# Kernel optimization log

Measured on AMD Instinct MI355X. Metric: run time of the kernel, lower is better.

Reference implementation:

```python
import jax, jax.numpy as jnp
import numpy as np

N, H, F, E, K = 2048, 1024, 4096, 8, 2


def setup_inputs() -> dict:
    key = jax.random.key(0)
    ks = jax.random.split(key, 6)
    x = jax.random.normal(ks[0], (N, H), dtype=jnp.float32)
    mapping = jax.random.randint(ks[1], (N, K), 0, E)
    Wg = jax.random.normal(ks[2], (E, H), dtype=jnp.float32) * (1.0 / np.sqrt(H))
    W1 = jax.random.normal(ks[3], (E, H, F), dtype=jnp.float32) * (1.0 / np.sqrt(H))
    b1 = jnp.zeros((E, F), dtype=jnp.float32)
    W2 = jax.random.normal(ks[4], (E, F, H), dtype=jnp.float32) * (1.0 / np.sqrt(F))
    b2 = jnp.zeros((E, H), dtype=jnp.float32)
    return {"x": x, "mapping": mapping, "Wg": Wg, "W1": W1, "b1": b1, "W2": W2, "b2": b2}


def reference(x, mapping, Wg, W1, b1, W2, b2):
    # Gate logits: note original applies softmax over dim=0 (the token axis).
    logits = jax.nn.softmax(x @ Wg.T, axis=0)  # [N, E]

    # Per-expert MLP. Original sorts tokens by expert, runs per-expert GEMMs on
    # dynamic splits, then unsorts -- mathematically: y[i,k] = MLP_{mapping[i,k]}(x[i]).
    # JIT-friendly dense baseline: run every expert over all tokens, gather per token.
    def mlp(e):
        h = jax.nn.gelu(x @ W1[e] + b1[e])  # [N, F]
        return h @ W2[e] + b2[e]            # [N, H]

    y_all = jnp.stack([mlp(e) for e in range(E)])  # [E, N, H]

    # Gate weights gathered per (token, k), normalized over top-k.
    w = jnp.take_along_axis(logits, mapping, axis=1)  # [N, K]
    w = w / jnp.sum(w, axis=-1, keepdims=True)

    idx = jnp.arange(x.shape[0])
    out = jnp.zeros_like(x)
    for k in range(mapping.shape[1]):
        yk = y_all[mapping[:, k], idx]  # [N, H] gather per token's k-th expert
        out = out + yk * w[:, k:k + 1]
    return out
```

## Files before the change

### kernel.cpp

```cpp
#include <hip/hip_runtime.h>

#define N_TOK 2048
#define HD    1024
#define FD    4096
#define NE    8
#define SK2   8

typedef __attribute__((ext_vector_type(8))) short short8;
typedef __attribute__((ext_vector_type(4))) float floatx4;

__device__ __forceinline__ unsigned short f2bf(float f) {
  unsigned int u = __float_as_uint(f);
  u += 0x7fffu + ((u >> 16) & 1u);
  return (unsigned short)(u >> 16);
}

__device__ __forceinline__ void gl2lds16(const unsigned short* g, unsigned short* l) {
  __builtin_amdgcn_global_load_lds(
      (const __attribute__((address_space(1))) unsigned int*)g,
      (__attribute__((address_space(3))) unsigned int*)l, 16, 0, 0);
}

__device__ __forceinline__ float gelu_tanh(float x) {
  float t = 0.7978845608028654f * x * (1.0f + 0.044715f * x * x);
  return 0.5f * x * (1.0f + tanhf(t));
}

__device__ __forceinline__ int poff_of(const int* __restrict__ cnt, int e) {
  int o = 0;
  for (int i = 0; i < e; ++i) o += (cnt[i] + 127) & ~127;
  return o;
}

__global__ void k_gating(const float* __restrict__ x, const float* __restrict__ wg,
                         float* __restrict__ p) {
  int wave = threadIdx.x >> 6;
  int lane = threadIdx.x & 63;
  int n = blockIdx.x * 4 + wave;
  const float4* xr = (const float4*)(x + (size_t)n * HD);
  float4 xv[4];
  #pragma unroll
  for (int i = 0; i < 4; ++i) xv[i] = xr[lane + i * 64];
  for (int e = 0; e < NE; ++e) {
    const float4* wr = (const float4*)(wg + (size_t)e * HD);
    float s = 0.f;
    #pragma unroll
    for (int i = 0; i < 4; ++i) {
      float4 w4 = wr[lane + i * 64];
      s += xv[i].x * w4.x + xv[i].y * w4.y + xv[i].z * w4.z + xv[i].w * w4.w;
    }
    for (int o = 32; o > 0; o >>= 1) s += __shfl_xor(s, o, 64);
    if (lane == 0) p[e * N_TOK + n] = s;
  }
}

__global__ void k_softmax(float* __restrict__ p) {
  int e = blockIdx.x;
  float* col = p + e * N_TOK;
  __shared__ float red[256];
  int t = threadIdx.x;
  float m = -1e30f;
  for (int i = t; i < N_TOK; i += 256) m = fmaxf(m, col[i]);
  red[t] = m; __syncthreads();
  for (int s = 128; s > 0; s >>= 1) { if (t < s) red[t] = fmaxf(red[t], red[t + s]); __syncthreads(); }
  m = red[0]; __syncthreads();
  float sum = 0.f;
  for (int i = t; i < N_TOK; i += 256) { float v = expf(col[i] - m); col[i] = v; sum += v; }
  red[t] = sum; __syncthreads();
  for (int s = 128; s > 0; s >>= 1) { if (t < s) red[t] += red[t + s]; __syncthreads(); }
  float inv = 1.0f / red[0];
  for (int i = t; i < N_TOK; i += 256) col[i] *= inv;
}

__global__ void k_route(const int* __restrict__ mp, const float* __restrict__ p,
                        int* __restrict__ cnt, int* __restrict__ idxl, float* __restrict__ wtl) {
  int n = blockIdx.x * 256 + threadIdx.x;
  if (n >= N_TOK) return;
  int m0 = mp[n * 2 + 0], m1 = mp[n * 2 + 1];
  if (m0 == m1) {
    int s = atomicAdd(&cnt[m0], 1);
    idxl[m0 * N_TOK + s] = n; wtl[m0 * N_TOK + s] = 1.0f;
  } else {
    float p0 = p[m0 * N_TOK + n], p1 = p[m1 * N_TOK + n];
    float inv = 1.0f / (p0 + p1);
    int s0 = atomicAdd(&cnt[m0], 1);
    idxl[m0 * N_TOK + s0] = n; wtl[m0 * N_TOK + s0] = p0 * inv;
    int s1 = atomicAdd(&cnt[m1], 1);
    idxl[m1 * N_TOK + s1] = n; wtl[m1 * N_TOK + s1] = p1 * inv;
  }
}

__global__ void k_gather(const float* __restrict__ x, const int* __restrict__ cnt,
                         const int* __restrict__ idxl, unsigned short* __restrict__ xg) {
  int e = blockIdx.y;
  int r = blockIdx.x;
  int c = cnt[e];
  int pc = (c + 127) & ~127;
  if (r >= pc) return;
  unsigned short* dst = xg + ((size_t)poff_of(cnt, e) + r) * HD;
  int t = threadIdx.x;
  union { unsigned short us[8]; uint4 v; } o;
  if (r < c) {
    const float* src = x + (size_t)idxl[e * N_TOK + r] * HD;
    float4 f0 = ((const float4*)src)[t * 2];
    float4 f1 = ((const float4*)src)[t * 2 + 1];
    o.us[0] = f2bf(f0.x); o.us[1] = f2bf(f0.y); o.us[2] = f2bf(f0.z); o.us[3] = f2bf(f0.w);
    o.us[4] = f2bf(f1.x); o.us[5] = f2bf(f1.y); o.us[6] = f2bf(f1.z); o.us[7] = f2bf(f1.w);
  } else {
    o.v.x = 0u; o.v.y = 0u; o.v.z = 0u; o.v.w = 0u;
  }
  ((uint4*)dst)[t] = o.v;
}

__global__ __launch_bounds__(256) void k_transcvt2(const float* __restrict__ w1,
                                                   unsigned short* __restrict__ w1t,
                                                   const float* __restrict__ w2,
                                                   unsigned short* __restrict__ w2t) {
  __shared__ float tile[64][65];
  int l = blockIdx.x;
  const float* src; unsigned short* dst; int rows, cols, bx, by, e;
  if (l < 8192) {
    src = w1; dst = w1t; rows = HD; cols = FD;
    bx = l & 63; by = (l >> 6) & 15; e = l >> 10;
  } else {
    int l2 = l - 8192;
    src = w2; dst = w2t; rows = FD; cols = HD;
    bx = l2 & 15; by = (l2 >> 4) & 63; e = l2 >> 10;
  }
  const size_t base = (size_t)e * rows * cols;
  int c0 = bx * 64, r0 = by * 64;
  int t = threadIdx.x;
  int lr = t >> 4;
  int lc = (t & 15) * 4;
  #pragma unroll
  for (int i = 0; i < 64; i += 16) {
    float4 v = *(const float4*)(src + base + (size_t)(r0 + lr + i) * cols + c0 + lc);
    tile[lr + i][lc] = v.x; tile[lr + i][lc + 1] = v.y;
    tile[lr + i][lc + 2] = v.z; tile[lr + i][lc + 3] = v.w;
  }
  __syncthreads();
  int oc = t >> 2;
  int rseg = (t & 3) * 16;
  union { unsigned short us[16]; uint4 v[2]; } o;
  #pragma unroll
  for (int i = 0; i < 16; ++i) o.us[i] = f2bf(tile[rseg + i][oc]);
  unsigned short* d = dst + base + (size_t)(c0 + oc) * rows + r0 + rseg;
  ((uint4*)d)[0] = o.v[0];
  ((uint4*)d)[1] = o.v[1];
}

__global__ __launch_bounds__(256) void k_gemm1(
    const unsigned short* __restrict__ xg, const unsigned short* __restrict__ w1t,
    const float* __restrict__ b1, const int* __restrict__ cnt,
    unsigned short* __restrict__ h) {
  const int l = blockIdx.x;
  const int r = l & 7;
  const int m = (l >> 3) & 31;
  const int q = l >> 8;
  const int e = q >> 2;
  const int n = ((q & 3) << 3) | r;

  const int c = cnt[e];
  const int mbase = m * 64;
  if (mbase >= c) return;
  const int nbase = n * 128;
  const int po = poff_of(cnt, e);
  const unsigned short* A = xg + ((size_t)po + mbase) * HD;
  const unsigned short* B = w1t + ((size_t)e * FD + nbase) * HD;

  __shared__ unsigned short As[64 * 32];
  __shared__ unsigned short Bs[128 * 32];

  const int tid = threadIdx.x;
  const int wave = tid >> 6, lane = tid & 63;
  const int quad = lane >> 4, lrow = lane & 15;
  const int wn = wave * 32;

  floatx4 acc[4][2];
  #pragma unroll
  for (int i = 0; i < 4; ++i)
    #pragma unroll
    for (int j = 0; j < 2; ++j) acc[i][j] = (floatx4){0.f, 0.f, 0.f, 0.f};

  const int rA = tid >> 2, kA = (tid & 3) * 8;
  const int rB0 = tid >> 2, kB0 = (tid & 3) * 8;
  const int rB1 = (256 + tid) >> 2, kB1 = ((256 + tid) & 3) * 8;

  for (int kt = 0; kt < HD / 32; ++kt) {
    __syncthreads();
    const unsigned short* ga = A + kt * 32;
    const unsigned short* gb = B + kt * 32;
    gl2lds16(ga + (size_t)rA * HD + kA, As + (size_t)(wave * 64) * 8);
    gl2lds16(gb + (size_t)rB0 * HD + kB0, Bs + (size_t)(wave * 64) * 8);
    gl2lds16(gb + (size_t)rB1 * HD + kB1, Bs + (size_t)(256 + wave * 64) * 8);
    __syncthreads();
    short8 aF[4], bF[2];
    #pragma unroll
    for (int i = 0; i < 4; ++i) aF[i] = *(const short8*)(As + (i * 16 + lrow) * 32 + quad * 8);
    #pragma unroll
    for (int j = 0; j < 2; ++j) bF[j] = *(const short8*)(Bs + (wn + j * 16 + lrow) * 32 + quad * 8);
    #pragma unroll
    for (int i = 0; i < 4; ++i)
      #pragma unroll
      for (int j = 0; j < 2; ++j)
        acc[i][j] = __builtin_amdgcn_mfma_f32_16x16x32_bf16(aF[i], bF[j], acc[i][j], 0, 0, 0);
  }

  const size_t hrow0 = (size_t)po + mbase;
  #pragma unroll
  for (int i = 0; i < 4; ++i) {
    #pragma unroll
    for (int rr = 0; rr < 4; ++rr) {
      int row = i * 16 + quad * 4 + rr;
      unsigned short* hr = h + (hrow0 + row) * FD + nbase;
      #pragma unroll
      for (int j = 0; j < 2; ++j) {
        int col = wn + j * 16 + lrow;
        float v = acc[i][j][rr] + b1[e * FD + nbase + col];
        hr[col] = f2bf(gelu_tanh(v));
      }
    }
  }
}

__global__ __launch_bounds__(256) void k_gemm2(
    const unsigned short* __restrict__ h, const unsigned short* __restrict__ w2t,
    const float* __restrict__ b2, const int* __restrict__ cnt,
    const int* __restrict__ idxl, const float* __restrict__ wtl, float* __restrict__ out) {
  const int l = blockIdx.x;
  const int sk = l & 7;
  const int m = (l >> 3) & 15;
  const int n = (l >> 7) & 7;
  const int e = l >> 10;

  const int c = cnt[e];
  const int mbase = m * 128;
  if (mbase >= c) return;
  const int nbase = n * 128;
  const int KC = FD / SK2;
  const int po = poff_of(cnt, e);
  const unsigned short* A = h + ((size_t)po + mbase) * FD + sk * KC;
  const unsigned short* B = w2t + ((size_t)e * HD + nbase) * FD + sk * KC;

  __shared__ unsigned short As[128 * 32];
  __shared__ unsigned short Bs[128 * 32];

  const int tid = threadIdx.x;
  const int wave = tid >> 6, lane = tid & 63;
  const int quad = lane >> 4, lrow = lane & 15;
  const int wm = (wave >> 1) * 64, wn = (wave & 1) * 64;

  floatx4 acc[4][4];
  #pragma unroll
  for (int i = 0; i < 4; ++i)
    #pragma unroll
    for (int j = 0; j < 4; ++j) acc[i][j] = (floatx4){0.f, 0.f, 0.f, 0.f};

  const int r0c = tid >> 2,          k0c = (tid & 3) * 8;
  const int r1c = (256 + tid) >> 2,  k1c = ((256 + tid) & 3) * 8;

  for (int kt = 0; kt < KC / 32; ++kt) {
    __syncthreads();
    const unsigned short* ga = A + kt * 32;
    const unsigned short* gb = B + kt * 32;
    gl2lds16(ga + (size_t)r0c * FD + k0c, As + (size_t)(wave * 64) * 8);
    gl2lds16(ga + (size_t)r1c * FD + k1c, As + (size_t)(256 + wave * 64) * 8);
    gl2lds16(gb + (size_t)r0c * FD + k0c, Bs + (size_t)(wave * 64) * 8);
    gl2lds16(gb + (size_t)r1c * FD + k1c, Bs + (size_t)(256 + wave * 64) * 8);
    __syncthreads();
    short8 aF[4], bF[4];
    #pragma unroll
    for (int i = 0; i < 4; ++i) aF[i] = *(const short8*)(As + (wm + i * 16 + lrow) * 32 + quad * 8);
    #pragma unroll
    for (int j = 0; j < 4; ++j) bF[j] = *(const short8*)(Bs + (wn + j * 16 + lrow) * 32 + quad * 8);
    #pragma unroll
    for (int i = 0; i < 4; ++i)
      #pragma unroll
      for (int j = 0; j < 4; ++j)
        acc[i][j] = __builtin_amdgcn_mfma_f32_16x16x32_bf16(aF[i], bF[j], acc[i][j], 0, 0, 0);
  }

  #pragma unroll
  for (int i = 0; i < 4; ++i) {
    #pragma unroll
    for (int rr = 0; rr < 4; ++rr) {
      int row = wm + i * 16 + quad * 4 + rr;
      int gr = mbase + row;
      if (gr < c) {
        int tok = idxl[e * N_TOK + gr];
        float wgt = wtl[e * N_TOK + gr];
        float* orow = out + (size_t)tok * HD + nbase;
        #pragma unroll
        for (int j = 0; j < 4; ++j) {
          int col = wn + j * 16 + lrow;
          float bias = (sk == 0) ? b2[e * HD + nbase + col] : 0.0f;
          atomicAdd(orow + col, wgt * (acc[i][j][rr] + bias));
        }
      }
    }
  }
}

extern "C" void kernel_launch(void* const* d_in, const int* in_sizes, int n_in,
                              void* d_out, int out_size, void* d_ws, size_t ws_size,
                              hipStream_t stream) {
  const float* x  = (const float*)d_in[0];
  const int*   mp = (const int*)d_in[1];
  const float* wg = (const float*)d_in[2];
  const float* w1 = (const float*)d_in[3];
  const float* b1 = (const float*)d_in[4];
  const float* w2 = (const float*)d_in[5];
  const float* b2 = (const float*)d_in[6];
  float* out = (float*)d_out;
  char* ws = (char*)d_ws;

  float* p    = (float*)(ws + 0);
  int*   cnt  = (int*)(ws + 65536);
  int*   idxl = (int*)(ws + 66048);
  float* wtl  = (float*)(ws + 131584);
  unsigned short* w1t = (unsigned short*)(ws + 197120);
  unsigned short* w2t = (unsigned short*)(ws + 197120 + 67108864);
  unsigned short* xg  = (unsigned short*)(ws + 197120 + 2 * 67108864);
  unsigned short* h   = (unsigned short*)(ws + 197120 + 2 * 67108864 + 10485760);

  hipMemsetAsync(cnt, 0, 32, stream);
  hipMemsetAsync(d_out, 0, (size_t)out_size * 4, stream);

  k_gating<<<512, 256, 0, stream>>>(x, wg, p);
  k_softmax<<<NE, 256, 0, stream>>>(p);
  k_route<<<NE, 256, 0, stream>>>(mp, p, cnt, idxl, wtl);
  k_transcvt2<<<16384, 256, 0, stream>>>(w1, w1t, w2, w2t);
  k_gather<<<dim3(N_TOK, NE), 128, 0, stream>>>(x, cnt, idxl, xg);
  k_gemm1<<<8192, 256, 0, stream>>>(xg, w1t, b1, cnt, h);
  k_gemm2<<<8192, 256, 0, stream>>>(h, w2t, b2, cnt, idxl, wtl, out);
}
```

Baseline: 580.2 us.

## Replace split-K atomic GEMM2 with full-K bf16 output plus per-token combine kernel

The second expert GEMM no longer splits K eight ways and scatters with float atomics into the output. It now computes full-K 64x64 tiles over the packed expert rows, writes bf16 results to a staging buffer, and a new combine kernel gathers each token's two expert rows, adds bias and applies the gate weights. Routing now records per-token expert, slot and weight, and the output memset is dropped. This removes heavy atomic traffic and the memset, but gives up split-K parallelism, uses smaller tiles with less reuse, and adds a bf16 rounding of the expert outputs.

```diff
diff --git a/kernel.cpp b/kernel.cpp
--- a/kernel.cpp
+++ b/kernel.cpp
@@ -4,7 +4,6 @@
 #define HD    1024
 #define FD    4096
 #define NE    8
-#define SK2   8
 
 typedef __attribute__((ext_vector_type(8))) short short8;
 typedef __attribute__((ext_vector_type(4))) float floatx4;
@@ -73,20 +72,25 @@
 }
 
 __global__ void k_route(const int* __restrict__ mp, const float* __restrict__ p,
-                        int* __restrict__ cnt, int* __restrict__ idxl, float* __restrict__ wtl) {
+                        int* __restrict__ cnt, int* __restrict__ idxl,
+                        int* __restrict__ tke, int* __restrict__ tks, float* __restrict__ tkw) {
   int n = blockIdx.x * 256 + threadIdx.x;
   if (n >= N_TOK) return;
   int m0 = mp[n * 2 + 0], m1 = mp[n * 2 + 1];
   if (m0 == m1) {
     int s = atomicAdd(&cnt[m0], 1);
-    idxl[m0 * N_TOK + s] = n; wtl[m0 * N_TOK + s] = 1.0f;
+    idxl[m0 * N_TOK + s] = n;
+    tke[n * 2] = m0; tks[n * 2] = s; tkw[n * 2] = 1.0f;
+    tke[n * 2 + 1] = m0; tks[n * 2 + 1] = s; tkw[n * 2 + 1] = 0.0f;
   } else {
     float p0 = p[m0 * N_TOK + n], p1 = p[m1 * N_TOK + n];
     float inv = 1.0f / (p0 + p1);
     int s0 = atomicAdd(&cnt[m0], 1);
-    idxl[m0 * N_TOK + s0] = n; wtl[m0 * N_TOK + s0] = p0 * inv;
+    idxl[m0 * N_TOK + s0] = n;
+    tke[n * 2] = m0; tks[n * 2] = s0; tkw[n * 2] = p0 * inv;
     int s1 = atomicAdd(&cnt[m1], 1);
-    idxl[m1 * N_TOK + s1] = n; wtl[m1 * N_TOK + s1] = p1 * inv;
+    idxl[m1 * N_TOK + s1] = n;
+    tke[n * 2 + 1] = m1; tks[n * 2 + 1] = s1; tkw[n * 2 + 1] = p1 * inv;
   }
 }
 
@@ -225,80 +229,108 @@
 
 __global__ __launch_bounds__(256) void k_gemm2(
     const unsigned short* __restrict__ h, const unsigned short* __restrict__ w2t,
-    const float* __restrict__ b2, const int* __restrict__ cnt,
-    const int* __restrict__ idxl, const float* __restrict__ wtl, float* __restrict__ out) {
+    const int* __restrict__ cnt, unsigned short* __restrict__ ya) {
   const int l = blockIdx.x;
-  const int sk = l & 7;
-  const int m = (l >> 3) & 15;
-  const int n = (l >> 7) & 7;
-  const int e = l >> 10;
-
-  const int c = cnt[e];
-  const int mbase = m * 128;
-  if (mbase >= c) return;
-  const int nbase = n * 128;
-  const int KC = FD / SK2;
-  const int po = poff_of(cnt, e);
-  const unsigned short* A = h + ((size_t)po + mbase) * FD + sk * KC;
-  const unsigned short* B = w2t + ((size_t)e * HD + nbase) * FD + sk * KC;
-
-  __shared__ unsigned short As[128 * 32];
-  __shared__ unsigned short Bs[128 * 32];
+  const int nt = l & 15;
+  const int mt = l >> 4;
+  const int mbase = mt * 64;
+  const int nbase = nt * 64;
+
+  int e = -1, po = 0, ce = 0;
+  {
+    int o = 0;
+    #pragma unroll
+    for (int i = 0; i < NE; ++i) {
+      int ci = cnt[i];
+      int pc = (ci + 127) & ~127;
+      if (mbase >= o && mbase < o + pc) { e = i; po = o; ce = ci; }
+      o += pc;
+    }
+  }
+  if (e < 0) return;
+  if (mbase - po >= ce) return;
+
+  const unsigned short* A = h + (size_t)mbase * FD;
+  const unsigned short* B = w2t + ((size_t)e * HD + nbase) * FD;
+
+  __shared__ unsigned short As[64 * 64];
+  __shared__ unsigned short Bs[64 * 64];
 
   const int tid = threadIdx.x;
   const int wave = tid >> 6, lane = tid & 63;
   const int quad = lane >> 4, lrow = lane & 15;
-  const int wm = (wave >> 1) * 64, wn = (wave & 1) * 64;
-
-  floatx4 acc[4][4];
-  #pragma unroll
-  for (int i = 0; i < 4; ++i)
-    #pragma unroll
-    for (int j = 0; j < 4; ++j) acc[i][j] = (floatx4){0.f, 0.f, 0.f, 0.f};
-
-  const int r0c = tid >> 2,          k0c = (tid & 3) * 8;
-  const int r1c = (256 + tid) >> 2,  k1c = ((256 + tid) & 3) * 8;
-
-  for (int kt = 0; kt < KC / 32; ++kt) {
+  const int wm = (wave >> 1) * 32, wn = (wave & 1) * 32;
+
+  floatx4 acc[2][2];
+  #pragma unroll
+  for (int i = 0; i < 2; ++i)
+    #pragma unroll
+    for (int j = 0; j < 2; ++j) acc[i][j] = (floatx4){0.f, 0.f, 0.f, 0.f};
+
+  const int s0 = tid,        r0 = s0 >> 3, k0 = (s0 & 7) * 8;
+  const int s1 = 256 + tid,  r1 = s1 >> 3, k1 = (s1 & 7) * 8;
+
+  for (int kt = 0; kt < FD / 64; ++kt) {
     __syncthreads();
-    const unsigned short* ga = A + kt * 32;
-    const unsigned short* gb = B + kt * 32;
-    gl2lds16(ga + (size_t)r0c * FD + k0c, As + (size_t)(wave * 64) * 8);
-    gl2lds16(ga + (size_t)r1c * FD + k1c, As + (size_t)(256 + wave * 64) * 8);
-    gl2lds16(gb + (size_t)r0c * FD + k0c, Bs + (size_t)(wave * 64) * 8);
-    gl2lds16(gb + (size_t)r1c * FD + k1c, Bs + (size_t)(256 + wave * 64) * 8);
+    const unsigned short* ga = A + kt * 64;
+    const unsigned short* gb = B + kt * 64;
+    gl2lds16(ga + (size_t)r0 * FD + k0, As + (size_t)(wave * 64) * 8);
+    gl2lds16(ga + (size_t)r1 * FD + k1, As + (size_t)(256 + wave * 64) * 8);
+    gl2lds16(gb + (size_t)r0 * FD + k0, Bs + (size_t)(wave * 64) * 8);
+    gl2lds16(gb + (size_t)r1 * FD + k1, Bs + (size_t)(256 + wave * 64) * 8);
     __syncthreads();
-    short8 aF[4], bF[4];
-    #pragma unroll
-    for (int i = 0; i < 4; ++i) aF[i] = *(const short8*)(As + (wm + i * 16 + lrow) * 32 + quad * 8);
-    #pragma unroll
-    for (int j = 0; j < 4; ++j) bF[j] = *(const short8*)(Bs + (wn + j * 16 + lrow) * 32 + quad * 8);
-    #pragma unroll
-    for (int i = 0; i < 4; ++i)
-      #pragma unroll
-      for (int j = 0; j < 4; ++j)
-        acc[i][j] = __builtin_amdgcn_mfma_f32_16x16x32_bf16(aF[i], bF[j], acc[i][j], 0, 0, 0);
-  }
-
-  #pragma unroll
-  for (int i = 0; i < 4; ++i) {
+    #pragma unroll
+    for (int c = 0; c < 2; ++c) {
+      short8 aF[2], bF[2];
+      #pragma unroll
+      for (int i = 0; i < 2; ++i) aF[i] = *(const short8*)(As + (wm + i * 16 + lrow) * 64 + c * 32 + quad * 8);
+      #pragma unroll
+      for (int j = 0; j < 2; ++j) bF[j] = *(const short8*)(Bs + (wn + j * 16 + lrow) * 64 + c * 32 + quad * 8);
+      #pragma unroll
+      for (int i = 0; i < 2; ++i)
+        #pragma unroll
+        for (int j = 0; j < 2; ++j)
+          acc[i][j] = __builtin_amdgcn_mfma_f32_16x16x32_bf16(aF[i], bF[j], acc[i][j], 0, 0, 0);
+    }
+  }
+
+  #pragma unroll
+  for (int i = 0; i < 2; ++i) {
     #pragma unroll
     for (int rr = 0; rr < 4; ++rr) {
-      int row = wm + i * 16 + quad * 4 + rr;
-      int gr = mbase + row;
-      if (gr < c) {
-        int tok = idxl[e * N_TOK + gr];
-        float wgt = wtl[e * N_TOK + gr];
-        float* orow = out + (size_t)tok * HD + nbase;
-        #pragma unroll
-        for (int j = 0; j < 4; ++j) {
-          int col = wn + j * 16 + lrow;
-          float bias = (sk == 0) ? b2[e * HD + nbase + col] : 0.0f;
-          atomicAdd(orow + col, wgt * (acc[i][j][rr] + bias));
-        }
+      int row = mbase + wm + i * 16 + quad * 4 + rr;
+      unsigned short* yr = ya + (size_t)row * HD + nbase;
+      #pragma unroll
+      for (int j = 0; j < 2; ++j) {
+        int col = wn + j * 16 + lrow;
+        yr[col] = f2bf(acc[i][j][rr]);
       }
     }
   }
+}
+
+__global__ __launch_bounds__(256) void k_combine(
+    const unsigned short* __restrict__ ya, const float* __restrict__ b2,
+    const int* __restrict__ cnt, const int* __restrict__ tke,
+    const int* __restrict__ tks, const float* __restrict__ tkw,
+    float* __restrict__ out) {
+  int n = blockIdx.x;
+  int e0 = tke[n * 2], e1 = tke[n * 2 + 1];
+  int p0 = poff_of(cnt, e0) + tks[n * 2];
+  int p1 = poff_of(cnt, e1) + tks[n * 2 + 1];
+  float w0 = tkw[n * 2], w1 = tkw[n * 2 + 1];
+  int c = threadIdx.x * 4;
+  union { unsigned short us[4]; ushort2 u2[2]; unsigned long long ll; } y0, y1;
+  y0.ll = *(const unsigned long long*)(ya + (size_t)p0 * HD + c);
+  y1.ll = *(const unsigned long long*)(ya + (size_t)p1 * HD + c);
+  float4 bb0 = *(const float4*)(b2 + (size_t)e0 * HD + c);
+  float4 bb1 = *(const float4*)(b2 + (size_t)e1 * HD + c);
+  float4 o;
+  o.x = w0 * (__uint_as_float((unsigned)y0.us[0] << 16) + bb0.x) + w1 * (__uint_as_float((unsigned)y1.us[0] << 16) + bb1.x);
+  o.y = w0 * (__uint_as_float((unsigned)y0.us[1] << 16) + bb0.y) + w1 * (__uint_as_float((unsigned)y1.us[1] << 16) + bb1.y);
+  o.z = w0 * (__uint_as_float((unsigned)y0.us[2] << 16) + bb0.z) + w1 * (__uint_as_float((unsigned)y1.us[2] << 16) + bb1.z);
+  o.w = w0 * (__uint_as_float((unsigned)y0.us[3] << 16) + bb0.w) + w1 * (__uint_as_float((unsigned)y1.us[3] << 16) + bb1.w);
+  *(float4*)(out + (size_t)n * HD + c) = o;
 }
 
 extern "C" void kernel_launch(void* const* d_in, const int* in_sizes, int n_in,
@@ -317,20 +349,24 @@
   float* p    = (float*)(ws + 0);
   int*   cnt  = (int*)(ws + 65536);
   int*   idxl = (int*)(ws + 66048);
-  float* wtl  = (float*)(ws + 131584);
-  unsigned short* w1t = (unsigned short*)(ws + 197120);
-  unsigned short* w2t = (unsigned short*)(ws + 197120 + 67108864);
-  unsigned short* xg  = (unsigned short*)(ws + 197120 + 2 * 67108864);
-  unsigned short* h   = (unsigned short*)(ws + 197120 + 2 * 67108864 + 10485760);
+  int*   tke  = (int*)(ws + 131584);
+  int*   tks  = (int*)(ws + 147968);
+  float* tkw  = (float*)(ws + 164352);
+  size_t off = 180736;
+  unsigned short* w1t = (unsigned short*)(ws + off);  off += 67108864;
+  unsigned short* w2t = (unsigned short*)(ws + off);  off += 67108864;
+  unsigned short* xg  = (unsigned short*)(ws + off);  off += 10485760;
+  unsigned short* h   = (unsigned short*)(ws + off);  off += 41943040;
+  unsigned short* ya  = (unsigned short*)(ws + off);  off += 10485760;
 
   hipMemsetAsync(cnt, 0, 32, stream);
-  hipMemsetAsync(d_out, 0, (size_t)out_size * 4, stream);
 
   k_gating<<<512, 256, 0, stream>>>(x, wg, p);
   k_softmax<<<NE, 256, 0, stream>>>(p);
-  k_route<<<NE, 256, 0, stream>>>(mp, p, cnt, idxl, wtl);
+  k_route<<<NE, 256, 0, stream>>>(mp, p, cnt, idxl, tke, tks, tkw);
   k_transcvt2<<<16384, 256, 0, stream>>>(w1, w1t, w2, w2t);
   k_gather<<<dim3(N_TOK, NE), 128, 0, stream>>>(x, cnt, idxl, xg);
   k_gemm1<<<8192, 256, 0, stream>>>(xg, w1t, b1, cnt, h);
-  k_gemm2<<<8192, 256, 0, stream>>>(h, w2t, b2, cnt, idxl, wtl, out);
-}
+  k_gemm2<<<80 * 16, 256, 0, stream>>>(h, w2t, cnt, ya);
+  k_combine<<<N_TOK, 256, 0, stream>>>(ya, b2, cnt, tke, tks, tkw, out);
+}
```

After: 505.1 us. 12.9% less time.
